# Optimization experiments

Measured on AMD Instinct MI355X. Metric: run time of the kernel, lower is better.

## Reference

```python
import jax, jax.numpy as jnp
from jax import lax
import numpy as np

B, IN, J, S, F, O, C, KS = 8, 8, 8, 187, 64, 64, 67, 15


def _ln(x, eps=1e-5):
    m = jnp.mean(x, axis=-1, keepdims=True)
    v = jnp.mean((x - m) ** 2, axis=-1, keepdims=True)
    return (x - m) / jnp.sqrt(v + eps)


def setup_inputs() -> dict:
    key = jax.random.key(0)
    ks = jax.random.split(key, 8)
    x_in = jax.random.normal(ks[0], (B, IN, S, F), jnp.float32)
    proj_x_prev = jax.random.normal(ks[1], (B, IN, S, O), jnp.float32)
    lin = jnp.linspace(-1.0, 1.0, C, dtype=jnp.float32)
    spline_weights = jnp.broadcast_to(lin, (IN, J, C)) + 0.01 * jax.random.normal(ks[2], (IN, J, C), jnp.float32)
    tau = 0.1 * jax.random.normal(ks[3], (IN, J), jnp.float32) + 0.1
    temperature = jnp.asarray(1.0, jnp.float32)
    omiga = jnp.full((IN, J), 0.2, jnp.float32)
    W2 = jax.random.normal(ks[4], (J, F, O), jnp.float32) * (1.0 / np.sqrt(F))
    b_param = 0.02 * jax.random.normal(ks[5], (J, S, O), jnp.float32)
    ln_scale = jnp.ones((J, F), jnp.float32)
    ln_bias = jnp.zeros((J, F), jnp.float32)
    alpha = jnp.ones((J,), jnp.float32)
    beta = jnp.ones((J,), jnp.float32)
    theta = jnp.ones((J,), jnp.float32)
    gamma = jnp.ones((J,), jnp.float32)
    w3 = 0.1 * jax.random.normal(ks[6], (J, O, KS), jnp.float32)  # depthwise conv kernels
    return dict(x_in=x_in, proj_x_prev=proj_x_prev, spline_weights=spline_weights, tau=tau,
                temperature=temperature, omiga=omiga, W2=W2, b_param=b_param, ln_scale=ln_scale,
                ln_bias=ln_bias, alpha=alpha, beta=beta, theta=theta, gamma=gamma, w3=w3)


def reference(x_in, proj_x_prev, spline_weights, tau, temperature, omiga, W2, b_param,
              ln_scale, ln_bias, alpha, beta, theta, gamma, w3):
    b, in_n, seq, feat = x_in.shape
    out_n, nC = spline_weights.shape[1], spline_weights.shape[2]
    kk = w3.shape[-1]
    # --- cubic B-spline basis ---
    h = 2.0 / (nC - 1)
    grid = jnp.linspace(-1.0, 1.0, nC, dtype=x_in.dtype)
    max_val = jnp.max(jnp.abs(x_in)) + 1e-8
    xn = jnp.clip(x_in / max_val * 0.95, -0.99, 0.99)
    dist = jnp.abs(xn[..., None] - grid) / h  # [b,in,seq,feat,C]
    basis = jax.nn.relu(2.0 - dist) ** 3 / 6.0 - jax.nn.relu(1.0 - dist) ** 3 * (4.0 / 6.0)
    spline_mapping = jnp.einsum('bisfc,ijc->bijsf', basis, spline_weights)
    activated = spline_mapping + jnp.abs(omiga)[None, :, :, None, None] * x_in[:, :, None]
    # --- energy-threshold gating ---
    energies = jnp.mean(activated ** 2, axis=(-1, -2))  # [b,in,out]
    tau_a = jnp.abs(tau)[None]
    t_val = jnp.abs(temperature) * np.sqrt(seq / 256.0) + 1e-4
    sqrtE = jnp.sqrt(energies + 1e-8)
    mask = jax.nn.sigmoid((sqrtE - tau_a) / t_val)  # [b,in,out]
    mult = sqrtE / (tau_a + 1e-8)
    wp = proj_x_prev[:, :, None] * (mult * mask)[..., None, None]  # [b,in,out,seq,d]
    d = wp.shape[-1]
    mid = in_n // 2
    Kt = wp[:, 0::2].transpose(0, 2, 3, 1, 4).reshape(b, out_n, seq, mid * d)
    Qt = wp[:, 1::2].transpose(0, 2, 3, 1, 4).reshape(b, out_n, seq, mid * d)
    Kt, Qt = _ln(Kt), _ln(Qt)
    raw = jnp.einsum('bjse,bjte->bjst', Kt, Qt)
    W1 = jax.nn.softmax(raw / (np.sqrt(mid * d) * t_val), axis=-1)  # [b,out,seq,seq]
    combined = jnp.einsum('bijsf,bij->bjsf', activated, mask)  # [b,out,seq,feat]
    # --- SplineWeightLayer (vectorized over out_n) ---
    xln = _ln(combined) * ln_scale[None, :, None, :] + ln_bias[None, :, None, :]
    x_prime = jnp.einsum('bjsh,jho->bjso', xln, W2) + b_param[None]  # [b,out,seq,O]
    o = x_prime.shape[-1]
    xt = x_prime.transpose(0, 2, 1, 3).reshape(b, seq, out_n * o)
    ker = w3.transpose(2, 0, 1).reshape(kk, 1, out_n * o)
    w3f = lax.conv_general_dilated(xt, ker, (1,), [(kk // 2, kk // 2)],
                                   dimension_numbers=('NWC', 'WIO', 'NWC'),
                                   feature_group_count=out_n * o)
    w3f = w3f.reshape(b, seq, out_n, o).transpose(0, 2, 1, 3)
    eye = jnp.eye(seq, dtype=x_in.dtype)
    attn_kernel = jnp.abs(beta)[None, :, None, None] * W1 + jnp.abs(alpha)[None, :, None, None] * eye
    global_part = jnp.einsum('bjst,bjto->bjso', attn_kernel, x_prime)
    spatial = global_part + jnp.abs(theta)[None, :, None, None] * w3f
    out = spatial + gamma[None, :, None, None] * combined  # residual_proj is Identity (F==O)
    return out, x_prime
```

## Files before the change

### kernel.cpp

```cpp
#include <hip/hip_runtime.h>
#include <math.h>

#define B_N 8
#define IN_N 8
#define J_N 8
#define S_N 187
#define F_N 64
#define O_N 64
#define C_N 67
#define KS_N 15
#define SF_N (S_N * F_N)
#define SF4_N (SF_N / 4)
#define SQRT_SF 0.85467470f

#define NT_SPL 12
#define NCOMB 384
#define NKT16 768
#define NRF 768
#define NMAXP 256
#define FRAG_BJ 49152
#define W1STRIDE 196

typedef __attribute__((ext_vector_type(8))) _Float16 half8;
typedef __attribute__((ext_vector_type(4))) _Float16 half4;
typedef __attribute__((ext_vector_type(4))) float floatx4;

__device__ __forceinline__ float wave_sum(float v) {
#pragma unroll
  for (int off = 32; off > 0; off >>= 1) v += __shfl_down(v, off, 64);
  return __shfl(v, 0, 64);
}
__device__ __forceinline__ float wave_max(float v) {
#pragma unroll
  for (int off = 32; off > 0; off >>= 1) v = fmaxf(v, __shfl_down(v, off, 64));
  return __shfl(v, 0, 64);
}
__device__ __forceinline__ float bspline(float d) {
  float t2 = fmaxf(2.f - d, 0.f);
  float t1 = fmaxf(1.f - d, 0.f);
  return t2 * t2 * t2 * (1.f / 6.f) - t1 * t1 * t1 * (4.f / 6.f);
}
__device__ __forceinline__ float get_inv095(const float* __restrict__ maxp) {
  int lane = threadIdx.x & 63;
  float m = 0.f;
#pragma unroll
  for (int k = 0; k < NMAXP / 64; k++) m = fmaxf(m, maxp[lane + k * 64]);
  return 0.95f / (wave_max(m) + 1e-8f);
}
__device__ __forceinline__ float gate_g(const float* __restrict__ esum_p, int bi, int j,
                                        const float* __restrict__ tau, float tv) {
  const float* p = esum_p + ((long)bi * 8 + j) * NT_SPL;
  float s = 0.f;
#pragma unroll
  for (int k = 0; k < NT_SPL; k++) s += p[k];
  float sE = sqrtf(s * (1.f / (float)SF_N) + 1e-8f);
  float ta = fabsf(tau[(bi & 7) * 8 + j]);
  return (sE / (ta + 1e-8f)) / (1.f + expf(-(sE - ta) / tv));
}

__global__ void k_maxabs(const float4* __restrict__ x, float* __restrict__ maxp, int n4) {
  __shared__ float red[4];
  int tid = blockIdx.x * 256 + threadIdx.x;
  float m = 0.f;
  for (int i = tid; i < n4; i += gridDim.x * 256) {
    float4 v = x[i];
    m = fmaxf(m, fmaxf(fmaxf(fabsf(v.x), fabsf(v.y)), fmaxf(fabsf(v.z), fabsf(v.w))));
  }
  m = wave_max(m);
  if ((threadIdx.x & 63) == 0) red[threadIdx.x >> 6] = m;
  __syncthreads();
  if (threadIdx.x == 0)
    maxp[blockIdx.x] = fmaxf(fmaxf(red[0], red[1]), fmaxf(red[2], red[3]));
}

__global__ void k_spline(const float4* __restrict__ x4, const float* __restrict__ sw,
                         const float* __restrict__ omiga, const float* __restrict__ maxp,
                         float4* __restrict__ act4, float* __restrict__ esum_p) {
  int tile = blockIdx.x, bi = blockIdx.y;
  int i = bi & 7;
  __shared__ float wl[C_N * 8];
  __shared__ float aom[J_N];
  __shared__ float red[4 * J_N];
  for (int t = threadIdx.x; t < J_N * C_N; t += 256) {
    int j = t / C_N, c = t - j * C_N;
    wl[c * 8 + j] = sw[i * J_N * C_N + t];
  }
  if (threadIdx.x < J_N) aom[threadIdx.x] = fabsf(omiga[i * J_N + threadIdx.x]);
  int lane = threadIdx.x & 63, wid = threadIdx.x >> 6;
  float inv = get_inv095(maxp);
  __syncthreads();
  int i4 = tile * 256 + threadIdx.x;
  float e[J_N] = {0, 0, 0, 0, 0, 0, 0, 0};
  if (i4 < SF4_N) {
    float4 xv = x4[(long)bi * SF4_N + i4];
    float xs[4] = {xv.x, xv.y, xv.z, xv.w};
    float4 av[J_N];
#pragma unroll
    for (int c = 0; c < 4; c++) {
      float x = xs[c];
      float xn = fminf(fmaxf(x * inv, -0.99f), 0.99f);
      float u = (xn + 1.f) * 33.f;
      int c0 = (int)floorf(u) - 1;
      float sm[J_N] = {0, 0, 0, 0, 0, 0, 0, 0};
#pragma unroll
      for (int kk = 0; kk < 4; kk++) {
        int cc = c0 + kk;
        if (cc >= 0 && cc < C_N) {
          float bas = bspline(fabsf(u - (float)cc));
          const float4* wp = (const float4*)(wl + cc * 8);
          float4 wa = wp[0], wb = wp[1];
          sm[0] += bas * wa.x; sm[1] += bas * wa.y;
          sm[2] += bas * wa.z; sm[3] += bas * wa.w;
          sm[4] += bas * wb.x; sm[5] += bas * wb.y;
          sm[6] += bas * wb.z; sm[7] += bas * wb.w;
        }
      }
#pragma unroll
      for (int j = 0; j < J_N; j++) {
        float a = sm[j] + aom[j] * x;
        (&av[j].x)[c] = a;
        e[j] += a * a;
      }
    }
#pragma unroll
    for (int j = 0; j < J_N; j++) act4[((long)(bi * 8 + j)) * SF4_N + i4] = av[j];
  }
#pragma unroll
  for (int j = 0; j < J_N; j++) {
    float v = e[j];
#pragma unroll
    for (int off = 32; off > 0; off >>= 1) v += __shfl_down(v, off, 64);
    if (lane == 0) red[wid * J_N + j] = v;
  }
  __syncthreads();
  if (threadIdx.x < J_N)
    esum_p[((long)bi * 8 + threadIdx.x) * NT_SPL + tile] =
        red[threadIdx.x] + red[8 + threadIdx.x] + red[16 + threadIdx.x] + red[24 + threadIdx.x];
}

__global__ void k_mid2(const float4* __restrict__ act4, const float* __restrict__ esum_p,
                       const float* __restrict__ tau, const float* __restrict__ temp,
                       const float* __restrict__ proj, const float* __restrict__ W2,
                       const float* __restrict__ bparam, const float* __restrict__ lns,
                       const float* __restrict__ lnb, float4* __restrict__ comb4,
                       float* __restrict__ xprime,
                       _Float16* __restrict__ khi, _Float16* __restrict__ klo,
                       _Float16* __restrict__ qhi, _Float16* __restrict__ qlo) {
  __shared__ float smem[8192 + 16 + 256];
  int lane = threadIdx.x & 63;
  if (blockIdx.x < NCOMB) {
    int blk = blockIdx.x;
    int tile = blk % 12, bjg = blk / 12;
    int jg = bjg & 3, b = bjg >> 2;
    int j0 = jg * 2;
    float* w2s = smem;
    float* mk  = smem + 8192;
    float* lss = smem + 8208;
    float* lbs = smem + 8336;
    {
      const float4* wg = (const float4*)(W2 + j0 * 4096);
      float4* ws4 = (float4*)w2s;
      for (int t = threadIdx.x; t < 2048; t += 256) ws4[t] = wg[t];
    }
    if (threadIdx.x < 128) {
      int jj = threadIdx.x >> 6, f = threadIdx.x & 63;
      lss[threadIdx.x] = lns[(j0 + jj) * 64 + f];
      lbs[threadIdx.x] = lnb[(j0 + jj) * 64 + f];
    }
    if (threadIdx.x < 16) {
      int i = threadIdx.x >> 1, j = j0 + (threadIdx.x & 1);
      const float* p = esum_p + ((long)(b * 8 + i) * 8 + j) * NT_SPL;
      float s = 0.f;
#pragma unroll
      for (int k = 0; k < NT_SPL; k++) s += p[k];
      float sE = sqrtf(s * (1.f / (float)SF_N) + 1e-8f);
      float ta = fabsf(tau[i * 8 + j]);
      float tv = fabsf(temp[0]) * SQRT_SF + 1e-4f;
      mk[threadIdx.x] = 1.f / (1.f + expf(-(sE - ta) / tv));
    }
    __syncthreads();
    int i4 = tile * 256 + threadIdx.x;
    if (i4 < SF4_N) {
      float4 cb[2] = {};
#pragma unroll
      for (int i = 0; i < IN_N; i++) {
#pragma unroll
        for (int jj = 0; jj < 2; jj++) {
          float4 a = act4[((long)((b * 8 + i) * 8 + j0 + jj)) * SF4_N + i4];
          float g = mk[i * 2 + jj];
          cb[jj].x += g * a.x; cb[jj].y += g * a.y;
          cb[jj].z += g * a.z; cb[jj].w += g * a.w;
        }
      }
#pragma unroll
      for (int jj = 0; jj < 2; jj++)
        comb4[((long)(b * J_N + j0 + jj)) * SF4_N + i4] = cb[jj];
      int s = i4 >> 4;
      int fx = (threadIdx.x & 15) * 4;
      int g0 = lane & 48;
#pragma unroll
      for (int jj = 0; jj < 2; jj++) {
        float4 c = cb[jj];
        float ls = c.x + c.y + c.z + c.w;
#pragma unroll
        for (int m = 1; m <= 8; m <<= 1) ls += __shfl_xor(ls, m, 64);
        float mean = ls * (1.f / 64.f);
        float d0 = c.x - mean, d1 = c.y - mean, d2 = c.z - mean, d3 = c.w - mean;
        float lv = d0 * d0 + d1 * d1 + d2 * d2 + d3 * d3;
#pragma unroll
        for (int m = 1; m <= 8; m <<= 1) lv += __shfl_xor(lv, m, 64);
        float invsd = 1.f / sqrtf(lv * (1.f / 64.f) + 1e-5f);
        float xln0 = d0 * invsd * lss[jj * 64 + fx + 0] + lbs[jj * 64 + fx + 0];
        float xln1 = d1 * invsd * lss[jj * 64 + fx + 1] + lbs[jj * 64 + fx + 1];
        float xln2 = d2 * invsd * lss[jj * 64 + fx + 2] + lbs[jj * 64 + fx + 2];
        float xln3 = d3 * invsd * lss[jj * 64 + fx + 3] + lbs[jj * 64 + fx + 3];
        float4 bp = *(const float4*)(bparam + ((long)(j0 + jj) * S_N + s) * 64 + fx);
        float a0 = bp.x, a1 = bp.y, a2 = bp.z, a3 = bp.w;
#pragma unroll
        for (int t16 = 0; t16 < 16; t16++) {
          int src = g0 + t16;
          float h0 = __shfl(xln0, src, 64);
          float h1 = __shfl(xln1, src, 64);
          float h2 = __shfl(xln2, src, 64);
          float h3 = __shfl(xln3, src, 64);
          const float* wrow = w2s + jj * 4096 + (t16 * 4) * 64 + fx;
          float4 w0 = *(const float4*)(wrow);
          float4 w1 = *(const float4*)(wrow + 64);
          float4 w2v = *(const float4*)(wrow + 128);
          float4 w3v = *(const float4*)(wrow + 192);
          a0 += h0 * w0.x + h1 * w1.x + h2 * w2v.x + h3 * w3v.x;
          a1 += h0 * w0.y + h1 * w1.y + h2 * w2v.y + h3 * w3v.y;
          a2 += h0 * w0.z + h1 * w1.z + h2 * w2v.z + h3 * w3v.z;
          a3 += h0 * w0.w + h1 * w1.w + h2 * w2v.w + h3 * w3v.w;
        }
        float4 o4 = {a0, a1, a2, a3};
        *(float4*)(xprime + (((long)(b * J_N + j0 + jj)) * S_N + s) * 64 + fx) = o4;
      }
    }
  } else {
    _Float16* stg = (_Float16*)smem;
    int blk = blockIdx.x - NCOMB;
    int bj = blk / 12, stile = blk - bj * 12;
    int b = bj >> 3, j = bj & 7;
    int w = threadIdx.x >> 6;
    int ig = lane >> 4;
    int f4 = (lane & 15) * 4;
    int iK = b * 8 + 2 * ig, iQ = iK + 1;
    float tv = fabsf(temp[0]) * SQRT_SF + 1e-4f;
    float gK = gate_g(esum_p, iK, j, tau, tv);
    float gQ = gate_g(esum_p, iQ, j, tau, tv);
    int slotbase = (lane >> 3) * 512 + ((lane >> 1) & 3) * 128 + (lane & 1) * 4;
    for (int rr = 0; rr < 4; rr++) {
      int m16 = w * 4 + rr;
      int s = stile * 16 + m16;
      half4 hk4 = {}, lk4 = {}, hq4 = {}, lq4 = {};
      if (s < S_N) {
        float4 kr = *(const float4*)(proj + ((long)iK * S_N + s) * 64 + f4);
        float4 qr = *(const float4*)(proj + ((long)iQ * S_N + s) * 64 + f4);
        float kv[4] = {kr.x * gK, kr.y * gK, kr.z * gK, kr.w * gK};
        float qv[4] = {qr.x * gQ, qr.y * gQ, qr.z * gQ, qr.w * gQ};
        float mkv = wave_sum(kv[0] + kv[1] + kv[2] + kv[3]) * (1.f / 256.f);
        float mqv = wave_sum(qv[0] + qv[1] + qv[2] + qv[3]) * (1.f / 256.f);
        float vk = 0.f, vq = 0.f;
#pragma unroll
        for (int q = 0; q < 4; q++) {
          float dk = kv[q] - mkv; vk += dk * dk;
          float dq = qv[q] - mqv; vq += dq * dq;
        }
        vk = wave_sum(vk) * (1.f / 256.f);
        vq = wave_sum(vq) * (1.f / 256.f);
        float ik = 1.f / sqrtf(vk + 1e-5f);
        float iq = 1.f / sqrtf(vq + 1e-5f);
#pragma unroll
        for (int q = 0; q < 4; q++) {
          float fk = (kv[q] - mkv) * ik;
          float fq = (qv[q] - mqv) * iq;
          _Float16 hk = (_Float16)fk;
          _Float16 hq = (_Float16)fq;
          hk4[q] = hk; lk4[q] = (_Float16)(fk - (float)hk);
          hq4[q] = hq; lq4[q] = (_Float16)(fq - (float)hq);
        }
      }
      int off = slotbase + m16 * 8;
      *(half4*)&stg[0 * 4096 + off] = hk4;
      *(half4*)&stg[1 * 4096 + off] = lk4;
      *(half4*)&stg[2 * 4096 + off] = hq4;
      *(half4*)&stg[3 * 4096 + off] = lq4;
    }
    __syncthreads();
    long gb = ((long)bj * 12 + stile) * 4096;
    float4* dk = (float4*)(khi + gb);
    float4* dkl = (float4*)(klo + gb);
    float4* dq = (float4*)(qhi + gb);
    float4* dql = (float4*)(qlo + gb);
    const float4* s0 = (const float4*)(stg + 0 * 4096);
    const float4* s1 = (const float4*)(stg + 1 * 4096);
    const float4* s2 = (const float4*)(stg + 2 * 4096);
    const float4* s3 = (const float4*)(stg + 3 * 4096);
    int t = threadIdx.x;
    dk[t] = s0[t];  dk[t + 256] = s0[t + 256];
    dkl[t] = s1[t]; dkl[t + 256] = s1[t + 256];
    dq[t] = s2[t];  dq[t + 256] = s2[t + 256];
    dql[t] = s3[t]; dql[t + 256] = s3[t + 256];
  }
}

__global__ void k_rawfinal(const _Float16* __restrict__ khi, const _Float16* __restrict__ klo,
                           const _Float16* __restrict__ qhi, const _Float16* __restrict__ qlo,
                           const float* __restrict__ temp, const float* __restrict__ xprime,
                           const float* __restrict__ comb, const float* __restrict__ w3,
                           const float* __restrict__ alpha, const float* __restrict__ beta,
                           const float* __restrict__ theta, const float* __restrict__ gamma,
                           float* __restrict__ out) {
  __shared__ float w1t[16 * W1STRIDE];
  __shared__ float w3s[16 * 64];
  int xcd = blockIdx.x & 7;
  int idx = blockIdx.x >> 3;
  int bj = xcd * 8 + idx / 12;
  int stile = idx - (idx / 12) * 12;
  int j = bj & 7;
  int w = threadIdx.x >> 6, lane = threadIdx.x & 63;
  int quad = lane >> 4, m16 = lane & 15;
  long fb = (long)bj * FRAG_BJ + lane * 8;
  for (int t = threadIdx.x; t < 16 * 64; t += 256) {
    int k = t >> 6, o = t & 63;
    w3s[t] = (k < KS_N) ? w3[j * 64 * KS_N + o * KS_N + k] : 0.f;
  }
  for (int t = threadIdx.x; t < 16 * 9; t += 256) {
    int r = t / 9, c = 187 + (t - r * 9);
    w1t[r * W1STRIDE + c] = 0.f;
  }
  const _Float16* ah_p = khi + fb + (long)stile * 4096;
  const _Float16* al_p = klo + fb + (long)stile * 4096;
  floatx4 acc[3] = {};
  for (int ec = 0; ec < 8; ec++) {
    half8 ah = *(const half8*)(ah_p + ec * 512);
    half8 al = *(const half8*)(al_p + ec * 512);
#pragma unroll
    for (int n = 0; n < 3; n++) {
      long bo = fb + (long)(w * 3 + n) * 4096 + ec * 512;
      half8 bh = *(const half8*)(qhi + bo);
      half8 bl = *(const half8*)(qlo + bo);
      acc[n] = __builtin_amdgcn_mfma_f32_16x16x32_f16(ah, bh, acc[n], 0, 0, 0);
      acc[n] = __builtin_amdgcn_mfma_f32_16x16x32_f16(al, bh, acc[n], 0, 0, 0);
      acc[n] = __builtin_amdgcn_mfma_f32_16x16x32_f16(ah, bl, acc[n], 0, 0, 0);
    }
  }
  float tv = fabsf(temp[0]) * SQRT_SF + 1e-4f;
  float scale = 1.f / (16.f * tv);
#pragma unroll
  for (int n = 0; n < 3; n++) {
    int t = (w * 3 + n) * 16 + m16;
    if (t < S_N) {
#pragma unroll
      for (int r = 0; r < 4; r++)
        w1t[(quad * 4 + r) * W1STRIDE + t] = acc[n][r] * scale;
    }
  }
  __syncthreads();
  int o = lane;
#pragma unroll
  for (int rr = 0; rr < 4; rr++) {
    float* row = &w1t[(w * 4 + rr) * W1STRIDE];
    float v[3];
    float m = -1e30f;
#pragma unroll
    for (int q = 0; q < 3; q++) {
      int t = o + q * 64;
      v[q] = (t < S_N) ? row[t] : -1e30f;
      m = fmaxf(m, v[q]);
    }
    m = wave_max(m);
    float ssum = 0.f;
#pragma unroll
    for (int q = 0; q < 3; q++) {
      int t = o + q * 64;
      float e = (t < S_N) ? expf(v[q] - m) : 0.f;
      v[q] = e;
      ssum += e;
    }
    ssum = wave_sum(ssum);
    float invs = 1.f / ssum;
#pragma unroll
    for (int q = 0; q < 3; q++) {
      int t = o + q * 64;
      if (t < S_N) row[t] = v[q] * invs;
    }
  }
  __syncthreads();
  int h = lane >> 5, o2 = lane & 31;
  int o0 = o2 * 2;
  const float* xpg = xprime + (long)bj * (S_N * 64);
  float aa = fabsf(alpha[j]), ba = fabsf(beta[j]), ta = fabsf(theta[j]), gv = gamma[j];
  int s0 = stile * 16;
  int tbase = h * 96;
  float ax[4] = {0.f, 0.f, 0.f, 0.f}, ay[4] = {0.f, 0.f, 0.f, 0.f};
  for (int tb = 0; tb < 96; tb += 4) {
    float4 wv[4];
#pragma unroll
    for (int rr = 0; rr < 4; rr++)
      wv[rr] = *(const float4*)&w1t[(w * 4 + rr) * W1STRIDE + tbase + tb];
#pragma unroll
    for (int q = 0; q < 4; q++) {
      int t = tbase + tb + q;
      int tc = (t < S_N) ? t : S_N - 1;
      float2 xv = *(const float2*)(xpg + tc * 64 + o0);
      float w0 = ((const float*)&wv[0])[q];
      float w1 = ((const float*)&wv[1])[q];
      float w2 = ((const float*)&wv[2])[q];
      float w3q = ((const float*)&wv[3])[q];
      ax[0] += w0 * xv.x; ay[0] += w0 * xv.y;
      ax[1] += w1 * xv.x; ay[1] += w1 * xv.y;
      ax[2] += w2 * xv.x; ay[2] += w2 * xv.y;
      ax[3] += w3q * xv.x; ay[3] += w3q * xv.y;
    }
  }
  float cx[4] = {0.f, 0.f, 0.f, 0.f}, cy[4] = {0.f, 0.f, 0.f, 0.f};
#pragma unroll
  for (int k = 0; k < 8; k++) {
    int kk = h * 8 + k;
    float2 wv3 = *(const float2*)&w3s[kk * 64 + o0];
#pragma unroll
    for (int rr = 0; rr < 4; rr++) {
      int si = s0 + w * 4 + rr + kk - 7;
      int sc = si < 0 ? 0 : (si >= S_N ? S_N - 1 : si);
      float2 xv = *(const float2*)(xpg + sc * 64 + o0);
      bool ok = (si >= 0) && (si < S_N);
      cx[rr] += ok ? wv3.x * xv.x : 0.f;
      cy[rr] += ok ? wv3.y * xv.y : 0.f;
    }
  }
#pragma unroll
  for (int rr = 0; rr < 4; rr++) {
    float px = ba * ax[rr] + ta * cx[rr];
    float py = ba * ay[rr] + ta * cy[rr];
    px += __shfl_xor(px, 32, 64);
    py += __shfl_xor(py, 32, 64);
    int s = s0 + w * 4 + rr;
    if (s < S_N) {
      float2 xs = *(const float2*)(xpg + s * 64 + o0);
      float2 cv = *(const float2*)(comb + ((long)bj * S_N + s) * 64 + o0);
      float2 res;
      res.x = px + aa * xs.x + gv * cv.x;
      res.y = py + aa * xs.y + gv * cv.y;
      if ((h == 0) == (rr < 2))
        *(float2*)(out + ((long)bj * S_N + s) * 64 + o0) = res;
    }
  }
}

extern "C" void kernel_launch(void* const* d_in, const int* in_sizes, int n_in,
                              void* d_out, int out_size, void* d_ws, size_t ws_size,
                              hipStream_t stream) {
  const float* x_in   = (const float*)d_in[0];
  const float* proj   = (const float*)d_in[1];
  const float* sw     = (const float*)d_in[2];
  const float* tau    = (const float*)d_in[3];
  const float* temp   = (const float*)d_in[4];
  const float* omiga  = (const float*)d_in[5];
  const float* W2     = (const float*)d_in[6];
  const float* bparam = (const float*)d_in[7];
  const float* lns    = (const float*)d_in[8];
  const float* lnb    = (const float*)d_in[9];
  const float* alpha  = (const float*)d_in[10];
  const float* beta   = (const float*)d_in[11];
  const float* theta  = (const float*)d_in[12];
  const float* gamma  = (const float*)d_in[13];
  const float* w3     = (const float*)d_in[14];

  float* out = (float*)d_out;
  float* xprime = out + B_N * J_N * S_N * O_N;

  float* wsf = (float*)d_ws;
  float* maxp   = wsf;
  float* esum_p = wsf + 512;
  float* act    = wsf + 512 + 512 * NT_SPL;
  const long ACT_N = (long)64 * 8 * SF_N;
  const long FR = (long)64 * FRAG_BJ;
  _Float16* khi = (_Float16*)(act + ACT_N);
  _Float16* klo = khi + FR;
  _Float16* qhi = klo + FR;
  _Float16* qlo = qhi + FR;
  float* comb = (float*)(qlo + FR);

  k_maxabs<<<NMAXP, 256, 0, stream>>>((const float4*)x_in, maxp, (B_N * IN_N * S_N * F_N) / 4);
  k_spline<<<dim3(NT_SPL, 64), 256, 0, stream>>>((const float4*)x_in, sw, omiga, maxp,
                                                 (float4*)act, esum_p);
  k_mid2<<<NCOMB + NKT16, 256, 0, stream>>>((const float4*)act, esum_p, tau, temp, proj,
                                            W2, bparam, lns, lnb, (float4*)comb, xprime,
                                            khi, klo, qhi, qlo);
  k_rawfinal<<<NRF, 256, 0, stream>>>(khi, klo, qhi, qlo, temp, xprime, comb,
                                      w3, alpha, beta, theta, gamma, out);
}
```

Measured before the change: 146.3 us.

## Fuse four pipeline kernels into one cooperative persistent kernel with grid syncs

Merges the maxabs, spline, combine/x_prime/K-Q staging and final attention kernels into a single cooperative launch of 768 blocks, separated by grid-wide barriers. Each former kernel body becomes a device function, and the K/Q staging blocks now handle two tiles each so the work fits the fixed grid. The goal is to remove inter-kernel launch gaps and tail drain. In exchange it adds grid.sync overhead, forces all stages to share one register and shared-memory budget with launch_bounds(256,3), and falls back to the four separate launches if the cooperative launch fails.

Result: slower. 421.9 us (+188.3%).

```diff
diff --git a/kernel.cpp b/kernel.cpp
--- a/kernel.cpp
+++ b/kernel.cpp
@@ -1,5 +1,8 @@
 #include <hip/hip_runtime.h>
+#include <hip/hip_cooperative_groups.h>
 #include <math.h>
+
+namespace cg = cooperative_groups;
 
 #define B_N 8
 #define IN_N 8
@@ -18,8 +21,10 @@
 #define NKT16 768
 #define NRF 768
 #define NMAXP 256
+#define NMEGA 768
 #define FRAG_BJ 49152
 #define W1STRIDE 196
+#define SMEM_F 8464
 
 typedef __attribute__((ext_vector_type(8))) _Float16 half8;
 typedef __attribute__((ext_vector_type(4))) _Float16 half4;
@@ -40,11 +45,10 @@
   float t1 = fmaxf(1.f - d, 0.f);
   return t2 * t2 * t2 * (1.f / 6.f) - t1 * t1 * t1 * (4.f / 6.f);
 }
-__device__ __forceinline__ float get_inv095(const float* __restrict__ maxp) {
+__device__ __forceinline__ float inv_from_partials(const float* __restrict__ maxp, int n) {
   int lane = threadIdx.x & 63;
   float m = 0.f;
-#pragma unroll
-  for (int k = 0; k < NMAXP / 64; k++) m = fmaxf(m, maxp[lane + k * 64]);
+  for (int k = lane; k < n; k += 64) m = fmaxf(m, maxp[k]);
   return 0.95f / (wave_max(m) + 1e-8f);
 }
 __device__ __forceinline__ float gate_g(const float* __restrict__ esum_p, int bi, int j,
@@ -58,38 +62,24 @@
   return (sE / (ta + 1e-8f)) / (1.f + expf(-(sE - ta) / tv));
 }
 
-__global__ void k_maxabs(const float4* __restrict__ x, float* __restrict__ maxp, int n4) {
-  __shared__ float red[4];
-  int tid = blockIdx.x * 256 + threadIdx.x;
-  float m = 0.f;
-  for (int i = tid; i < n4; i += gridDim.x * 256) {
-    float4 v = x[i];
-    m = fmaxf(m, fmaxf(fmaxf(fabsf(v.x), fabsf(v.y)), fmaxf(fabsf(v.z), fabsf(v.w))));
-  }
-  m = wave_max(m);
-  if ((threadIdx.x & 63) == 0) red[threadIdx.x >> 6] = m;
-  __syncthreads();
-  if (threadIdx.x == 0)
-    maxp[blockIdx.x] = fmaxf(fmaxf(red[0], red[1]), fmaxf(red[2], red[3]));
-}
-
-__global__ void k_spline(const float4* __restrict__ x4, const float* __restrict__ sw,
-                         const float* __restrict__ omiga, const float* __restrict__ maxp,
-                         float4* __restrict__ act4, float* __restrict__ esum_p) {
-  int tile = blockIdx.x, bi = blockIdx.y;
+
+__device__ void spline_body(int tile, int bi, float inv, float* smem,
+                            const float4* __restrict__ x4, const float* __restrict__ sw,
+                            const float* __restrict__ omiga,
+                            float4* __restrict__ act4, float* __restrict__ esum_p) {
+  float* wl  = smem;
+  float* aom = smem + 536;
+  float* red = smem + 544;
+  int tid = threadIdx.x, lane = tid & 63, wid = tid >> 6;
   int i = bi & 7;
-  __shared__ float wl[C_N * 8];
-  __shared__ float aom[J_N];
-  __shared__ float red[4 * J_N];
-  for (int t = threadIdx.x; t < J_N * C_N; t += 256) {
+  __syncthreads();
+  for (int t = tid; t < J_N * C_N; t += 256) {
     int j = t / C_N, c = t - j * C_N;
     wl[c * 8 + j] = sw[i * J_N * C_N + t];
   }
-  if (threadIdx.x < J_N) aom[threadIdx.x] = fabsf(omiga[i * J_N + threadIdx.x]);
-  int lane = threadIdx.x & 63, wid = threadIdx.x >> 6;
-  float inv = get_inv095(maxp);
-  __syncthreads();
-  int i4 = tile * 256 + threadIdx.x;
+  if (tid < J_N) aom[tid] = fabsf(omiga[i * J_N + tid]);
+  __syncthreads();
+  int i4 = tile * 256 + tid;
   float e[J_N] = {0, 0, 0, 0, 0, 0, 0, 0};
   if (i4 < SF4_N) {
     float4 xv = x4[(long)bi * SF4_N + i4];
@@ -133,195 +123,199 @@
     if (lane == 0) red[wid * J_N + j] = v;
   }
   __syncthreads();
-  if (threadIdx.x < J_N)
-    esum_p[((long)bi * 8 + threadIdx.x) * NT_SPL + tile] =
-        red[threadIdx.x] + red[8 + threadIdx.x] + red[16 + threadIdx.x] + red[24 + threadIdx.x];
-}
-
-__global__ void k_mid2(const float4* __restrict__ act4, const float* __restrict__ esum_p,
-                       const float* __restrict__ tau, const float* __restrict__ temp,
-                       const float* __restrict__ proj, const float* __restrict__ W2,
-                       const float* __restrict__ bparam, const float* __restrict__ lns,
-                       const float* __restrict__ lnb, float4* __restrict__ comb4,
-                       float* __restrict__ xprime,
-                       _Float16* __restrict__ khi, _Float16* __restrict__ klo,
-                       _Float16* __restrict__ qhi, _Float16* __restrict__ qlo) {
-  __shared__ float smem[8192 + 16 + 256];
+  if (tid < J_N)
+    esum_p[((long)bi * 8 + tid) * NT_SPL + tile] =
+        red[tid] + red[8 + tid] + red[16 + tid] + red[24 + tid];
+}
+
+__device__ void comb_xp_body(int blk, float* smem, const float4* __restrict__ act4,
+                             const float* __restrict__ esum_p, const float* __restrict__ tau,
+                             const float* __restrict__ temp, const float* __restrict__ W2,
+                             const float* __restrict__ bparam, const float* __restrict__ lns,
+                             const float* __restrict__ lnb, float4* __restrict__ comb4,
+                             float* __restrict__ xprime) {
   int lane = threadIdx.x & 63;
-  if (blockIdx.x < NCOMB) {
-    int blk = blockIdx.x;
-    int tile = blk % 12, bjg = blk / 12;
-    int jg = bjg & 3, b = bjg >> 2;
-    int j0 = jg * 2;
-    float* w2s = smem;
-    float* mk  = smem + 8192;
-    float* lss = smem + 8208;
-    float* lbs = smem + 8336;
-    {
-      const float4* wg = (const float4*)(W2 + j0 * 4096);
-      float4* ws4 = (float4*)w2s;
-      for (int t = threadIdx.x; t < 2048; t += 256) ws4[t] = wg[t];
-    }
-    if (threadIdx.x < 128) {
-      int jj = threadIdx.x >> 6, f = threadIdx.x & 63;
-      lss[threadIdx.x] = lns[(j0 + jj) * 64 + f];
-      lbs[threadIdx.x] = lnb[(j0 + jj) * 64 + f];
-    }
-    if (threadIdx.x < 16) {
-      int i = threadIdx.x >> 1, j = j0 + (threadIdx.x & 1);
-      const float* p = esum_p + ((long)(b * 8 + i) * 8 + j) * NT_SPL;
-      float s = 0.f;
-#pragma unroll
-      for (int k = 0; k < NT_SPL; k++) s += p[k];
-      float sE = sqrtf(s * (1.f / (float)SF_N) + 1e-8f);
-      float ta = fabsf(tau[i * 8 + j]);
-      float tv = fabsf(temp[0]) * SQRT_SF + 1e-4f;
-      mk[threadIdx.x] = 1.f / (1.f + expf(-(sE - ta) / tv));
-    }
-    __syncthreads();
-    int i4 = tile * 256 + threadIdx.x;
-    if (i4 < SF4_N) {
-      float4 cb[2] = {};
-#pragma unroll
-      for (int i = 0; i < IN_N; i++) {
-#pragma unroll
-        for (int jj = 0; jj < 2; jj++) {
-          float4 a = act4[((long)((b * 8 + i) * 8 + j0 + jj)) * SF4_N + i4];
-          float g = mk[i * 2 + jj];
-          cb[jj].x += g * a.x; cb[jj].y += g * a.y;
-          cb[jj].z += g * a.z; cb[jj].w += g * a.w;
-        }
+  int tile = blk % 12, bjg = blk / 12;
+  int jg = bjg & 3, b = bjg >> 2;
+  int j0 = jg * 2;
+  float* w2s = smem;
+  float* mk  = smem + 8192;
+  float* lss = smem + 8208;
+  float* lbs = smem + 8336;
+  __syncthreads();
+  {
+    const float4* wg = (const float4*)(W2 + j0 * 4096);
+    float4* ws4 = (float4*)w2s;
+    for (int t = threadIdx.x; t < 2048; t += 256) ws4[t] = wg[t];
+  }
+  if (threadIdx.x < 128) {
+    int jj = threadIdx.x >> 6, f = threadIdx.x & 63;
+    lss[threadIdx.x] = lns[(j0 + jj) * 64 + f];
+    lbs[threadIdx.x] = lnb[(j0 + jj) * 64 + f];
+  }
+  if (threadIdx.x < 16) {
+    int i = threadIdx.x >> 1, j = j0 + (threadIdx.x & 1);
+    const float* p = esum_p + ((long)(b * 8 + i) * 8 + j) * NT_SPL;
+    float s = 0.f;
+#pragma unroll
+    for (int k = 0; k < NT_SPL; k++) s += p[k];
+    float sE = sqrtf(s * (1.f / (float)SF_N) + 1e-8f);
+    float ta = fabsf(tau[i * 8 + j]);
+    float tv = fabsf(temp[0]) * SQRT_SF + 1e-4f;
+    mk[threadIdx.x] = 1.f / (1.f + expf(-(sE - ta) / tv));
+  }
+  __syncthreads();
+  int i4 = tile * 256 + threadIdx.x;
+  if (i4 < SF4_N) {
+    float4 cb[2] = {};
+#pragma unroll
+    for (int i = 0; i < IN_N; i++) {
+#pragma unroll
+      for (int jj = 0; jj < 2; jj++) {
+        float4 a = act4[((long)((b * 8 + i) * 8 + j0 + jj)) * SF4_N + i4];
+        float g = mk[i * 2 + jj];
+        cb[jj].x += g * a.x; cb[jj].y += g * a.y;
+        cb[jj].z += g * a.z; cb[jj].w += g * a.w;
       }
-#pragma unroll
-      for (int jj = 0; jj < 2; jj++)
-        comb4[((long)(b * J_N + j0 + jj)) * SF4_N + i4] = cb[jj];
-      int s = i4 >> 4;
-      int fx = (threadIdx.x & 15) * 4;
-      int g0 = lane & 48;
-#pragma unroll
-      for (int jj = 0; jj < 2; jj++) {
-        float4 c = cb[jj];
-        float ls = c.x + c.y + c.z + c.w;
-#pragma unroll
-        for (int m = 1; m <= 8; m <<= 1) ls += __shfl_xor(ls, m, 64);
-        float mean = ls * (1.f / 64.f);
-        float d0 = c.x - mean, d1 = c.y - mean, d2 = c.z - mean, d3 = c.w - mean;
-        float lv = d0 * d0 + d1 * d1 + d2 * d2 + d3 * d3;
-#pragma unroll
-        for (int m = 1; m <= 8; m <<= 1) lv += __shfl_xor(lv, m, 64);
-        float invsd = 1.f / sqrtf(lv * (1.f / 64.f) + 1e-5f);
-        float xln0 = d0 * invsd * lss[jj * 64 + fx + 0] + lbs[jj * 64 + fx + 0];
-        float xln1 = d1 * invsd * lss[jj * 64 + fx + 1] + lbs[jj * 64 + fx + 1];
-        float xln2 = d2 * invsd * lss[jj * 64 + fx + 2] + lbs[jj * 64 + fx + 2];
-        float xln3 = d3 * invsd * lss[jj * 64 + fx + 3] + lbs[jj * 64 + fx + 3];
-        float4 bp = *(const float4*)(bparam + ((long)(j0 + jj) * S_N + s) * 64 + fx);
-        float a0 = bp.x, a1 = bp.y, a2 = bp.z, a3 = bp.w;
-#pragma unroll
-        for (int t16 = 0; t16 < 16; t16++) {
-          int src = g0 + t16;
-          float h0 = __shfl(xln0, src, 64);
-          float h1 = __shfl(xln1, src, 64);
-          float h2 = __shfl(xln2, src, 64);
-          float h3 = __shfl(xln3, src, 64);
-          const float* wrow = w2s + jj * 4096 + (t16 * 4) * 64 + fx;
-          float4 w0 = *(const float4*)(wrow);
-          float4 w1 = *(const float4*)(wrow + 64);
-          float4 w2v = *(const float4*)(wrow + 128);
-          float4 w3v = *(const float4*)(wrow + 192);
-          a0 += h0 * w0.x + h1 * w1.x + h2 * w2v.x + h3 * w3v.x;
-          a1 += h0 * w0.y + h1 * w1.y + h2 * w2v.y + h3 * w3v.y;
-          a2 += h0 * w0.z + h1 * w1.z + h2 * w2v.z + h3 * w3v.z;
-          a3 += h0 * w0.w + h1 * w1.w + h2 * w2v.w + h3 * w3v.w;
-        }
-        float4 o4 = {a0, a1, a2, a3};
-        *(float4*)(xprime + (((long)(b * J_N + j0 + jj)) * S_N + s) * 64 + fx) = o4;
+    }
+#pragma unroll
+    for (int jj = 0; jj < 2; jj++)
+      comb4[((long)(b * J_N + j0 + jj)) * SF4_N + i4] = cb[jj];
+    int s = i4 >> 4;
+    int fx = (threadIdx.x & 15) * 4;
+    int g0 = lane & 48;
+#pragma unroll
+    for (int jj = 0; jj < 2; jj++) {
+      float4 c = cb[jj];
+      float ls = c.x + c.y + c.z + c.w;
+#pragma unroll
+      for (int m = 1; m <= 8; m <<= 1) ls += __shfl_xor(ls, m, 64);
+      float mean = ls * (1.f / 64.f);
+      float d0 = c.x - mean, d1 = c.y - mean, d2 = c.z - mean, d3 = c.w - mean;
+      float lv = d0 * d0 + d1 * d1 + d2 * d2 + d3 * d3;
+#pragma unroll
+      for (int m = 1; m <= 8; m <<= 1) lv += __shfl_xor(lv, m, 64);
+      float invsd = 1.f / sqrtf(lv * (1.f / 64.f) + 1e-5f);
+      float xln0 = d0 * invsd * lss[jj * 64 + fx + 0] + lbs[jj * 64 + fx + 0];
+      float xln1 = d1 * invsd * lss[jj * 64 + fx + 1] + lbs[jj * 64 + fx + 1];
+      float xln2 = d2 * invsd * lss[jj * 64 + fx + 2] + lbs[jj * 64 + fx + 2];
+      float xln3 = d3 * invsd * lss[jj * 64 + fx + 3] + lbs[jj * 64 + fx + 3];
+      float4 bp = *(const float4*)(bparam + ((long)(j0 + jj) * S_N + s) * 64 + fx);
+      float a0 = bp.x, a1 = bp.y, a2 = bp.z, a3 = bp.w;
+#pragma unroll
+      for (int t16 = 0; t16 < 16; t16++) {
+        int src = g0 + t16;
+        float h0 = __shfl(xln0, src, 64);
+        float h1 = __shfl(xln1, src, 64);
+        float h2 = __shfl(xln2, src, 64);
+        float h3 = __shfl(xln3, src, 64);
+        const float* wrow = w2s + jj * 4096 + (t16 * 4) * 64 + fx;
+        float4 w0 = *(const float4*)(wrow);
+        float4 w1 = *(const float4*)(wrow + 64);
+        float4 w2v = *(const float4*)(wrow + 128);
+        float4 w3v = *(const float4*)(wrow + 192);
+        a0 += h0 * w0.x + h1 * w1.x + h2 * w2v.x + h3 * w3v.x;
+        a1 += h0 * w0.y + h1 * w1.y + h2 * w2v.y + h3 * w3v.y;
+        a2 += h0 * w0.z + h1 * w1.z + h2 * w2v.z + h3 * w3v.z;
+        a3 += h0 * w0.w + h1 * w1.w + h2 * w2v.w + h3 * w3v.w;
       }
-    }
-  } else {
-    _Float16* stg = (_Float16*)smem;
-    int blk = blockIdx.x - NCOMB;
-    int bj = blk / 12, stile = blk - bj * 12;
-    int b = bj >> 3, j = bj & 7;
-    int w = threadIdx.x >> 6;
-    int ig = lane >> 4;
-    int f4 = (lane & 15) * 4;
-    int iK = b * 8 + 2 * ig, iQ = iK + 1;
-    float tv = fabsf(temp[0]) * SQRT_SF + 1e-4f;
-    float gK = gate_g(esum_p, iK, j, tau, tv);
-    float gQ = gate_g(esum_p, iQ, j, tau, tv);
-    int slotbase = (lane >> 3) * 512 + ((lane >> 1) & 3) * 128 + (lane & 1) * 4;
-    for (int rr = 0; rr < 4; rr++) {
-      int m16 = w * 4 + rr;
-      int s = stile * 16 + m16;
-      half4 hk4 = {}, lk4 = {}, hq4 = {}, lq4 = {};
-      if (s < S_N) {
-        float4 kr = *(const float4*)(proj + ((long)iK * S_N + s) * 64 + f4);
-        float4 qr = *(const float4*)(proj + ((long)iQ * S_N + s) * 64 + f4);
-        float kv[4] = {kr.x * gK, kr.y * gK, kr.z * gK, kr.w * gK};
-        float qv[4] = {qr.x * gQ, qr.y * gQ, qr.z * gQ, qr.w * gQ};
-        float mkv = wave_sum(kv[0] + kv[1] + kv[2] + kv[3]) * (1.f / 256.f);
-        float mqv = wave_sum(qv[0] + qv[1] + qv[2] + qv[3]) * (1.f / 256.f);
-        float vk = 0.f, vq = 0.f;
-#pragma unroll
-        for (int q = 0; q < 4; q++) {
-          float dk = kv[q] - mkv; vk += dk * dk;
-          float dq = qv[q] - mqv; vq += dq * dq;
-        }
-        vk = wave_sum(vk) * (1.f / 256.f);
-        vq = wave_sum(vq) * (1.f / 256.f);
-        float ik = 1.f / sqrtf(vk + 1e-5f);
-        float iq = 1.f / sqrtf(vq + 1e-5f);
-#pragma unroll
-        for (int q = 0; q < 4; q++) {
-          float fk = (kv[q] - mkv) * ik;
-          float fq = (qv[q] - mqv) * iq;
-          _Float16 hk = (_Float16)fk;
-          _Float16 hq = (_Float16)fq;
-          hk4[q] = hk; lk4[q] = (_Float16)(fk - (float)hk);
-          hq4[q] = hq; lq4[q] = (_Float16)(fq - (float)hq);
-        }
+      float4 o4 = {a0, a1, a2, a3};
+      *(float4*)(xprime + (((long)(b * J_N + j0 + jj)) * S_N + s) * 64 + fx) = o4;
+    }
+  }
+}
+
+__device__ void ktqt_body(int blk, float* smem, const float* __restrict__ esum_p,
+                          const float* __restrict__ tau, const float* __restrict__ temp,
+                          const float* __restrict__ proj,
+                          _Float16* __restrict__ khi, _Float16* __restrict__ klo,
+                          _Float16* __restrict__ qhi, _Float16* __restrict__ qlo) {
+  _Float16* stg = (_Float16*)smem;
+  int lane = threadIdx.x & 63;
+  int bj = blk / 12, stile = blk - bj * 12;
+  int b = bj >> 3, j = bj & 7;
+  int w = threadIdx.x >> 6;
+  int ig = lane >> 4;
+  int f4 = (lane & 15) * 4;
+  int iK = b * 8 + 2 * ig, iQ = iK + 1;
+  float tv = fabsf(temp[0]) * SQRT_SF + 1e-4f;
+  float gK = gate_g(esum_p, iK, j, tau, tv);
+  float gQ = gate_g(esum_p, iQ, j, tau, tv);
+  int slotbase = (lane >> 3) * 512 + ((lane >> 1) & 3) * 128 + (lane & 1) * 4;
+  __syncthreads();
+  for (int rr = 0; rr < 4; rr++) {
+    int m16 = w * 4 + rr;
+    int s = stile * 16 + m16;
+    half4 hk4 = {}, lk4 = {}, hq4 = {}, lq4 = {};
+    if (s < S_N) {
+      float4 kr = *(const float4*)(proj + ((long)iK * S_N + s) * 64 + f4);
+      float4 qr = *(const float4*)(proj + ((long)iQ * S_N + s) * 64 + f4);
+      float kv[4] = {kr.x * gK, kr.y * gK, kr.z * gK, kr.w * gK};
+      float qv[4] = {qr.x * gQ, qr.y * gQ, qr.z * gQ, qr.w * gQ};
+      float mkv = wave_sum(kv[0] + kv[1] + kv[2] + kv[3]) * (1.f / 256.f);
+      float mqv = wave_sum(qv[0] + qv[1] + qv[2] + qv[3]) * (1.f / 256.f);
+      float vk = 0.f, vq = 0.f;
+#pragma unroll
+      for (int q = 0; q < 4; q++) {
+        float dk = kv[q] - mkv; vk += dk * dk;
+        float dq = qv[q] - mqv; vq += dq * dq;
       }
-      int off = slotbase + m16 * 8;
-      *(half4*)&stg[0 * 4096 + off] = hk4;
-      *(half4*)&stg[1 * 4096 + off] = lk4;
-      *(half4*)&stg[2 * 4096 + off] = hq4;
-      *(half4*)&stg[3 * 4096 + off] = lq4;
-    }
-    __syncthreads();
-    long gb = ((long)bj * 12 + stile) * 4096;
-    float4* dk = (float4*)(khi + gb);
-    float4* dkl = (float4*)(klo + gb);
-    float4* dq = (float4*)(qhi + gb);
-    float4* dql = (float4*)(qlo + gb);
-    const float4* s0 = (const float4*)(stg + 0 * 4096);
-    const float4* s1 = (const float4*)(stg + 1 * 4096);
-    const float4* s2 = (const float4*)(stg + 2 * 4096);
-    const float4* s3 = (const float4*)(stg + 3 * 4096);
-    int t = threadIdx.x;
-    dk[t] = s0[t];  dk[t + 256] = s0[t + 256];
-    dkl[t] = s1[t]; dkl[t + 256] = s1[t + 256];
-    dq[t] = s2[t];  dq[t + 256] = s2[t + 256];
-    dql[t] = s3[t]; dql[t + 256] = s3[t + 256];
-  }
-}
-
-__global__ void k_rawfinal(const _Float16* __restrict__ khi, const _Float16* __restrict__ klo,
-                           const _Float16* __restrict__ qhi, const _Float16* __restrict__ qlo,
-                           const float* __restrict__ temp, const float* __restrict__ xprime,
-                           const float* __restrict__ comb, const float* __restrict__ w3,
-                           const float* __restrict__ alpha, const float* __restrict__ beta,
-                           const float* __restrict__ theta, const float* __restrict__ gamma,
-                           float* __restrict__ out) {
-  __shared__ float w1t[16 * W1STRIDE];
-  __shared__ float w3s[16 * 64];
-  int xcd = blockIdx.x & 7;
-  int idx = blockIdx.x >> 3;
+      vk = wave_sum(vk) * (1.f / 256.f);
+      vq = wave_sum(vq) * (1.f / 256.f);
+      float ik = 1.f / sqrtf(vk + 1e-5f);
+      float iq = 1.f / sqrtf(vq + 1e-5f);
+#pragma unroll
+      for (int q = 0; q < 4; q++) {
+        float fk = (kv[q] - mkv) * ik;
+        float fq = (qv[q] - mqv) * iq;
+        _Float16 hk = (_Float16)fk;
+        _Float16 hq = (_Float16)fq;
+        hk4[q] = hk; lk4[q] = (_Float16)(fk - (float)hk);
+        hq4[q] = hq; lq4[q] = (_Float16)(fq - (float)hq);
+      }
+    }
+    int off = slotbase + m16 * 8;
+    *(half4*)&stg[0 * 4096 + off] = hk4;
+    *(half4*)&stg[1 * 4096 + off] = lk4;
+    *(half4*)&stg[2 * 4096 + off] = hq4;
+    *(half4*)&stg[3 * 4096 + off] = lq4;
+  }
+  __syncthreads();
+  long gb = ((long)bj * 12 + stile) * 4096;
+  float4* dk = (float4*)(khi + gb);
+  float4* dkl = (float4*)(klo + gb);
+  float4* dq = (float4*)(qhi + gb);
+  float4* dql = (float4*)(qlo + gb);
+  const float4* s0 = (const float4*)(stg + 0 * 4096);
+  const float4* s1 = (const float4*)(stg + 1 * 4096);
+  const float4* s2 = (const float4*)(stg + 2 * 4096);
+  const float4* s3 = (const float4*)(stg + 3 * 4096);
+  int t = threadIdx.x;
+  dk[t] = s0[t];  dk[t + 256] = s0[t + 256];
+  dkl[t] = s1[t]; dkl[t + 256] = s1[t + 256];
+  dq[t] = s2[t];  dq[t + 256] = s2[t + 256];
+  dql[t] = s3[t]; dql[t + 256] = s3[t + 256];
+}
+
+__device__ void rawfinal_body(int bid, float* smem,
+                              const _Float16* __restrict__ khi, const _Float16* __restrict__ klo,
+                              const _Float16* __restrict__ qhi, const _Float16* __restrict__ qlo,
+                              const float* __restrict__ temp, const float* __restrict__ xprime,
+                              const float* __restrict__ comb, const float* __restrict__ w3,
+                              const float* __restrict__ alpha, const float* __restrict__ beta,
+                              const float* __restrict__ theta, const float* __restrict__ gamma,
+                              float* __restrict__ out) {
+  float* w1t = smem;
+  float* w3s = smem + 3136;
+  int xcd = bid & 7;
+  int idx = bid >> 3;
   int bj = xcd * 8 + idx / 12;
   int stile = idx - (idx / 12) * 12;
   int j = bj & 7;
   int w = threadIdx.x >> 6, lane = threadIdx.x & 63;
   int quad = lane >> 4, m16 = lane & 15;
   long fb = (long)bj * FRAG_BJ + lane * 8;
+  __syncthreads();
   for (int t = threadIdx.x; t < 16 * 64; t += 256) {
     int k = t >> 6, o = t & 63;
     w3s[t] = (k < KS_N) ? w3[j * 64 * KS_N + o * KS_N + k] : 0.f;
@@ -449,10 +443,92 @@
   }
 }
 
+__global__ __launch_bounds__(256, 3) void k_mega(
+    const float4* x4, const float* sw, const float* omiga, const float* tau,
+    const float* temp, const float* proj, const float* W2, const float* bparam,
+    const float* lns, const float* lnb, const float* w3, const float* alpha,
+    const float* beta, const float* theta, const float* gamma,
+    float* maxp, float* esum_p, float4* act4,
+    _Float16* khi, _Float16* klo, _Float16* qhi, _Float16* qlo,
+    float4* comb4, float* xprime, float* out) {
+  __shared__ float smem[SMEM_F];
+  cg::grid_group grid = cg::this_grid();
+  int bid = blockIdx.x, tid = threadIdx.x;
+  {
+    const int n4 = (B_N * IN_N * S_N * F_N) / 4;
+    float m = 0.f;
+    int i = bid * 256 + tid;
+    if (i < n4) {
+      float4 v = x4[i];
+      m = fmaxf(fmaxf(fabsf(v.x), fabsf(v.y)), fmaxf(fabsf(v.z), fabsf(v.w)));
+    }
+    m = wave_max(m);
+    if ((tid & 63) == 0) smem[tid >> 6] = m;
+    __syncthreads();
+    if (tid == 0) maxp[bid] = fmaxf(fmaxf(smem[0], smem[1]), fmaxf(smem[2], smem[3]));
+  }
+  grid.sync();
+  float inv = inv_from_partials(maxp, NMEGA);
+  spline_body(bid % 12, bid / 12, inv, smem, x4, sw, omiga, act4, esum_p);
+  grid.sync();
+  if (bid < NCOMB) {
+    comb_xp_body(bid, smem, act4, esum_p, tau, temp, W2, bparam, lns, lnb, comb4, xprime);
+  } else {
+    int base = (bid - NCOMB) * 2;
+    ktqt_body(base, smem, esum_p, tau, temp, proj, khi, klo, qhi, qlo);
+    ktqt_body(base + 1, smem, esum_p, tau, temp, proj, khi, klo, qhi, qlo);
+  }
+  grid.sync();
+  rawfinal_body(bid, smem, khi, klo, qhi, qlo, temp, xprime,
+                (const float*)comb4, w3, alpha, beta, theta, gamma, out);
+}
+
+__global__ void k_maxabs(const float4* __restrict__ x, float* __restrict__ maxp, int n4) {
+  __shared__ float red[4];
+  int tid = blockIdx.x * 256 + threadIdx.x;
+  float m = 0.f;
+  for (int i = tid; i < n4; i += gridDim.x * 256) {
+    float4 v = x[i];
+    m = fmaxf(m, fmaxf(fmaxf(fabsf(v.x), fabsf(v.y)), fmaxf(fabsf(v.z), fabsf(v.w))));
+  }
+  m = wave_max(m);
+  if ((threadIdx.x & 63) == 0) red[threadIdx.x >> 6] = m;
+  __syncthreads();
+  if (threadIdx.x == 0)
+    maxp[blockIdx.x] = fmaxf(fmaxf(red[0], red[1]), fmaxf(red[2], red[3]));
+}
+__global__ void k_spline(const float4* x4, const float* sw, const float* omiga,
+                         const float* maxp, float4* act4, float* esum_p) {
+  __shared__ float smem[576];
+  float inv = inv_from_partials(maxp, NMAXP);
+  spline_body(blockIdx.x, blockIdx.y, inv, smem, x4, sw, omiga, act4, esum_p);
+}
+__global__ void k_mid2(const float4* act4, const float* esum_p, const float* tau,
+                       const float* temp, const float* proj, const float* W2,
+                       const float* bparam, const float* lns, const float* lnb,
+                       float4* comb4, float* xprime,
+                       _Float16* khi, _Float16* klo, _Float16* qhi, _Float16* qlo) {
+  __shared__ float smem[SMEM_F];
+  if (blockIdx.x < NCOMB)
+    comb_xp_body(blockIdx.x, smem, act4, esum_p, tau, temp, W2, bparam, lns, lnb,
+                 comb4, xprime);
+  else
+    ktqt_body(blockIdx.x - NCOMB, smem, esum_p, tau, temp, proj, khi, klo, qhi, qlo);
+}
+__global__ void k_rawfinal(const _Float16* khi, const _Float16* klo, const _Float16* qhi,
+                           const _Float16* qlo, const float* temp, const float* xprime,
+                           const float* comb, const float* w3, const float* alpha,
+                           const float* beta, const float* theta, const float* gamma,
+                           float* out) {
+  __shared__ float smem[4160];
+  rawfinal_body(blockIdx.x, smem, khi, klo, qhi, qlo, temp, xprime, comb, w3,
+                alpha, beta, theta, gamma, out);
+}
+
 extern "C" void kernel_launch(void* const* d_in, const int* in_sizes, int n_in,
                               void* d_out, int out_size, void* d_ws, size_t ws_size,
                               hipStream_t stream) {
-  const float* x_in   = (const float*)d_in[0];
+  const float4* x4    = (const float4*)d_in[0];
   const float* proj   = (const float*)d_in[1];
   const float* sw     = (const float*)d_in[2];
   const float* tau    = (const float*)d_in[3];
@@ -473,8 +549,8 @@
 
   float* wsf = (float*)d_ws;
   float* maxp   = wsf;
-  float* esum_p = wsf + 512;
-  float* act    = wsf + 512 + 512 * NT_SPL;
+  float* esum_p = wsf + 768;
+  float* act    = wsf + 768 + 512 * NT_SPL;
   const long ACT_N = (long)64 * 8 * SF_N;
   const long FR = (long)64 * FRAG_BJ;
   _Float16* khi = (_Float16*)(act + ACT_N);
@@ -482,13 +558,22 @@
   _Float16* qhi = klo + FR;
   _Float16* qlo = qhi + FR;
   float* comb = (float*)(qlo + FR);
-
-  k_maxabs<<<NMAXP, 256, 0, stream>>>((const float4*)x_in, maxp, (B_N * IN_N * S_N * F_N) / 4);
-  k_spline<<<dim3(NT_SPL, 64), 256, 0, stream>>>((const float4*)x_in, sw, omiga, maxp,
-                                                 (float4*)act, esum_p);
-  k_mid2<<<NCOMB + NKT16, 256, 0, stream>>>((const float4*)act, esum_p, tau, temp, proj,
-                                            W2, bparam, lns, lnb, (float4*)comb, xprime,
-                                            khi, klo, qhi, qlo);
-  k_rawfinal<<<NRF, 256, 0, stream>>>(khi, klo, qhi, qlo, temp, xprime, comb,
-                                      w3, alpha, beta, theta, gamma, out);
-}
+  float4* act4 = (float4*)act;
+  float4* comb4 = (float4*)comb;
+
+  void* args[] = {&x4, &sw, &omiga, &tau, &temp, &proj, &W2, &bparam, &lns, &lnb,
+                  &w3, &alpha, &beta, &theta, &gamma, &maxp, &esum_p, &act4,
+                  &khi, &klo, &qhi, &qlo, &comb4, &xprime, &out};
+  hipError_t err = hipLaunchCooperativeKernel((const void*)k_mega, dim3(NMEGA), dim3(256),
+                                              args, 0, stream);
+  if (err != hipSuccess) {
+    (void)hipGetLastError();
+    k_maxabs<<<NMAXP, 256, 0, stream>>>(x4, maxp, (B_N * IN_N * S_N * F_N) / 4);
+    k_spline<<<dim3(NT_SPL, 64), 256, 0, stream>>>(x4, sw, omiga, maxp, act4, esum_p);
+    k_mid2<<<NCOMB + NKT16, 256, 0, stream>>>(act4, esum_p, tau, temp, proj, W2,
+                                              bparam, lns, lnb, comb4, xprime,
+                                              khi, klo, qhi, qlo);
+    k_rawfinal<<<NRF, 256, 0, stream>>>(khi, klo, qhi, qlo, temp, xprime, comb,
+                                        w3, alpha, beta, theta, gamma, out);
+  }
+}
```
